# Kernel tuning notes

Hardware: AMD Instinct MI355X
Metric: run time of the kernel (lower is better)

The kernel has to match this reference:

```python
import jax, jax.numpy as jnp
import numpy as np

N, C_IN, C_HID, C_OUT = 50000, 256, 64 * 4, 64
E = 1_600_000
P_DROP = 0.5


def setup_inputs() -> dict:
    key = jax.random.key(0)
    ks = jax.random.split(key, 12)
    cat = C_IN + C_HID  # DConv input is concat([X, H]) -> in+hidden channels
    glorot = lambda k, sh: jax.random.normal(k, sh, jnp.float32) * (2.0 / (sh[-2] + sh[-1])) ** 0.5
    inp = {
        "x": jax.random.normal(ks[0], (N, C_IN), jnp.float32),
        "edge_index": jax.random.randint(ks[1], (2, E), 0, N, jnp.int64),
        "edge_weight": jax.random.uniform(ks[2], (E,), jnp.float32),
        # deterministic dropout mask (training-mode dropout, p=0.5), pre-scaled by 1/(1-p)
        "mask": (jax.random.uniform(ks[3], (N, C_IN)) >= P_DROP).astype(jnp.float32) / (1.0 - P_DROP),
        # DConv weights: shape (2, K=1, in+hidden, hidden) per gate
        "w_z": glorot(ks[4], (2, 1, cat, C_HID)),
        "b_z": jnp.zeros((C_HID,), jnp.float32),
        "w_r": glorot(ks[5], (2, 1, cat, C_HID)),
        "b_r": jnp.zeros((C_HID,), jnp.float32),
        "w_h": glorot(ks[6], (2, 1, cat, C_HID)),
        "b_h": jnp.zeros((C_HID,), jnp.float32),
        "w_lin": glorot(ks[7], (C_OUT, C_HID)),
        "b_lin": jnp.zeros((C_OUT,), jnp.float32),
    }
    return inp


def _dconv(inp, w, b):
    # K=1 diffusion conv: only the zeroth-order (identity) term of both the
    # forward- and backward-transition expansions survives; edges are unused.
    return inp @ w[0, 0] + inp @ w[1, 0] + b


def reference(x, edge_index, edge_weight, mask, w_z, b_z, w_r, b_r, w_h, b_h, w_lin, b_lin):
    x = x * mask  # F.dropout, training=True, deterministic mask
    H = jnp.zeros((x.shape[0], w_z.shape[-1]), x.dtype)  # initial hidden state
    xh = jnp.concatenate([x, H], axis=1)                  # [N, in+hid]
    Z = jax.nn.sigmoid(_dconv(xh, w_z, b_z))              # update gate
    R = jax.nn.sigmoid(_dconv(xh, w_r, b_r))              # reset gate
    xhr = jnp.concatenate([x, H * R], axis=1)
    H_tilde = jnp.tanh(_dconv(xhr, w_h, b_h))             # candidate state
    H = Z * H + (1.0 - Z) * H_tilde                       # GRU blend
    h = jax.nn.elu(H)
    return h @ w_lin.T + b_lin                            # [N, out]
```

## Files before the change

kernel.cpp:

```cpp
#include <hip/hip_runtime.h>
#include <hip/hip_bf16.h>


typedef __attribute__((ext_vector_type(8))) short bf16x8;
typedef __attribute__((ext_vector_type(4))) float f32x4;

constexpr int N_ROWS = 50000;
constexpr int CIN  = 256;
constexpr int COUT = 64;
constexpr int BM   = 32;

__device__ inline unsigned short f2bf(float f) {
    union { float f; unsigned u; } v; v.f = f;
    unsigned r = v.u + 0x7fffu + ((v.u >> 16) & 1u);
    return (unsigned short)(r >> 16);
}
__device__ inline float bf2f(unsigned short b) {
    union { unsigned u; float f; } v; v.u = ((unsigned)b) << 16;
    return v.f;
}
__device__ inline f32x4 mfma16(bf16x8 a, bf16x8 b, f32x4 c) {
    return __builtin_amdgcn_mfma_f32_16x16x32_bf16(a, b, c, 0, 0, 0);
}
__device__ __forceinline__ void gload16(const void* g, void* l) {
    __builtin_amdgcn_global_load_lds(
        (const __attribute__((address_space(1))) char*)g,
        (__attribute__((address_space(3))) char*)l, 16, 0, 0);
}

__global__ __launch_bounds__(256) void prep_frags(
    const float* __restrict__ wz, const float* __restrict__ wh,
    const float* __restrict__ wlin, unsigned short* __restrict__ ws)
{
    int t = blockIdx.x * 256 + threadIdx.x;
    int frag = t >> 6, lane = t & 63;
    if (frag >= 288) return;
    int g16 = lane & 15, kg = lane >> 4;
    unsigned short vals[8];
    if (frag < 256) {
        int kb = frag & 7, nf = (frag >> 3) & 15, g = frag >> 7;
        const float* wsrc = g ? wh : wz;
        int n = nf * 16 + g16;
        #pragma unroll
        for (int j = 0; j < 8; ++j) {
            int k = kb * 32 + kg * 8 + j;
            float v = wsrc[k * 256 + n] + wsrc[131072 + k * 256 + n];
            vals[j] = f2bf(v);
        }
    } else {
        int f = frag - 256;
        int kb = f & 7, nf = f >> 3;
        int n = nf * 16 + g16;
        #pragma unroll
        for (int j = 0; j < 8; ++j) {
            int k = kb * 32 + kg * 8 + j;
            vals[j] = f2bf(wlin[n * 256 + k]);
        }
    }
    unsigned short* dst = ws + (size_t)frag * 512 + lane * 8;
    #pragma unroll
    for (int j = 0; j < 8; ++j) dst[j] = vals[j];
}

__global__ __launch_bounds__(512)
__attribute__((amdgpu_waves_per_eu(4, 4)))
void dcrnn_async(
    const float* __restrict__ x, const float* __restrict__ mask,
    const unsigned short* __restrict__ wf,
    const float* __restrict__ bz, const float* __restrict__ bh,
    const float* __restrict__ blin, float* __restrict__ out)
{
    __shared__ char smem[65536];
    char* AhiB = smem;
    char* AloB = smem + 16384;
    const int tid = threadIdx.x, lane = tid & 63, wv = tid >> 6;
    const int l16 = lane & 15, lk = lane >> 4;
    const int row0 = blockIdx.x * BM;
    const int nf0 = wv * 2;
    char* wbuf = smem + 32768 + wv * 4096;

    auto stage_gate = [&](int kb, int g) {
        char* dst = wbuf + g * 2048;
        gload16(wf + (size_t)((g * 16 + nf0)     * 8 + kb) * 512 + lane * 8, dst);
        gload16(wf + (size_t)((g * 16 + nf0 + 1) * 8 + kb) * 512 + lane * 8, dst + 1024);
    };
    auto stage_out = [&](int v) {
        char* dst = wbuf + (v & 1) * 2048;
        gload16(wf + (size_t)(256 + (wv & 3) * 8 + 2 * v)     * 512 + lane * 8, dst);
        gload16(wf + (size_t)(256 + (wv & 3) * 8 + 2 * v + 1) * 512 + lane * 8, dst + 1024);
    };

    stage_gate(0, 0);
    stage_gate(0, 1);

    float bzv[2], bhv[2];
    #pragma unroll
    for (int nfi = 0; nfi < 2; ++nfi) {
        int col = wv * 32 + nfi * 16 + l16;
        bzv[nfi] = bz[col]; bhv[nfi] = bh[col];
    }
    const int ocol = (wv & 3) * 16 + l16;
    const float bo = blin[ocol];
    const int mo = wv >> 2;

    #pragma unroll
    for (int it = 0; it < 4; ++it) {
        int s = it * 512 + tid, r = s >> 6, c4 = s & 63;
        int row = row0 + r;
        float4 xv = make_float4(0.f, 0.f, 0.f, 0.f), mv = xv;
        if (row < N_ROWS) {
            xv = reinterpret_cast<const float4*>(x    + (size_t)row * CIN)[c4];
            mv = reinterpret_cast<const float4*>(mask + (size_t)row * CIN)[c4];
        }
        float v0 = xv.x * mv.x, v1 = xv.y * mv.y, v2 = xv.z * mv.z, v3 = xv.w * mv.w;
        unsigned short h0 = f2bf(v0), h1 = f2bf(v1), h2 = f2bf(v2), h3 = f2bf(v3);
        unsigned short l0 = f2bf(v0 - bf2f(h0)), l1 = f2bf(v1 - bf2f(h1));
        unsigned short l2 = f2bf(v2 - bf2f(h2)), l3 = f2bf(v3 - bf2f(h3));
        int byte = ((r * CIN + c4 * 4) * 2) ^ ((r & 7) << 4);
        *reinterpret_cast<ushort4*>(AhiB + byte) = make_ushort4(h0, h1, h2, h3);
        *reinterpret_cast<ushort4*>(AloB + byte) = make_ushort4(l0, l1, l2, l3);
    }
    __syncthreads();

    f32x4 accZ[2][2], accH[2][2];
    #pragma unroll
    for (int nfi = 0; nfi < 2; ++nfi)
        #pragma unroll
        for (int m = 0; m < 2; ++m) {
            accZ[nfi][m] = (f32x4){0.f, 0.f, 0.f, 0.f};
            accH[nfi][m] = (f32x4){0.f, 0.f, 0.f, 0.f};
        }

    for (int kb = 0; kb < 8; ++kb) {
        bf16x8 ah[2], al[2];
        int koff = kb * 32 + lk * 8;
        #pragma unroll
        for (int m = 0; m < 2; ++m) {
            int row = m * 16 + l16;
            int byte = ((row * CIN + koff) * 2) ^ ((row & 7) << 4);
            ah[m] = *reinterpret_cast<const bf16x8*>(AhiB + byte);
            al[m] = *reinterpret_cast<const bf16x8*>(AloB + byte);
        }
        if (kb >= 1) asm volatile("s_waitcnt vmcnt(2)" ::: "memory");
        bf16x8 zb0 = *reinterpret_cast<const bf16x8*>(wbuf + lane * 16);
        bf16x8 zb1 = *reinterpret_cast<const bf16x8*>(wbuf + 1024 + lane * 16);
        asm volatile("s_waitcnt lgkmcnt(0)" ::: "memory");
        if (kb < 7) stage_gate(kb + 1, 0); else stage_out(0);
        #pragma unroll
        for (int m = 0; m < 2; ++m) {
            accZ[0][m] = mfma16(ah[m], zb0, accZ[0][m]);
            accZ[0][m] = mfma16(al[m], zb0, accZ[0][m]);
            accZ[1][m] = mfma16(ah[m], zb1, accZ[1][m]);
            accZ[1][m] = mfma16(al[m], zb1, accZ[1][m]);
        }
        if (kb >= 1) asm volatile("s_waitcnt vmcnt(2)" ::: "memory");
        bf16x8 hb0 = *reinterpret_cast<const bf16x8*>(wbuf + 2048 + lane * 16);
        bf16x8 hb1 = *reinterpret_cast<const bf16x8*>(wbuf + 3072 + lane * 16);
        asm volatile("s_waitcnt lgkmcnt(0)" ::: "memory");
        if (kb < 7) stage_gate(kb + 1, 1); else stage_out(1);
        #pragma unroll
        for (int m = 0; m < 2; ++m) {
            accH[0][m] = mfma16(ah[m], hb0, accH[0][m]);
            accH[0][m] = mfma16(al[m], hb0, accH[0][m]);
            accH[1][m] = mfma16(ah[m], hb1, accH[1][m]);
            accH[1][m] = mfma16(al[m], hb1, accH[1][m]);
        }
    }
    __syncthreads();

    #pragma unroll
    for (int nfi = 0; nfi < 2; ++nfi) {
        int col = wv * 32 + nfi * 16 + l16;
        #pragma unroll
        for (int m = 0; m < 2; ++m) {
            #pragma unroll
            for (int i = 0; i < 4; ++i) {
                float z  = 1.f / (1.f + __expf(-(accZ[nfi][m][i] + bzv[nfi])));
                float tt = __expf(2.f * (accH[nfi][m][i] + bhv[nfi]));
                float th = (tt - 1.f) / (tt + 1.f);
                float H  = (1.f - z) * th;
                float h  = (H > 0.f) ? H : (__expf(H) - 1.f);
                int row = m * 16 + lk * 4 + i;
                unsigned pk = ((unsigned)f2bf(h)) << 16;
                int byte = (row * 1024 + col * 4) ^ ((row & 7) << 4);
                *reinterpret_cast<unsigned*>(smem + byte) = pk;
            }
        }
    }
    __syncthreads();

    f32x4 accO = (f32x4){0.f, 0.f, 0.f, 0.f};
    for (int v = 0; v < 4; ++v) {
        if (v == 2) asm volatile("s_waitcnt vmcnt(2)" ::: "memory");
        if (v == 3) asm volatile("s_waitcnt vmcnt(0)" ::: "memory");
        bf16x8 cb0 = *reinterpret_cast<const bf16x8*>(wbuf + (v & 1) * 2048 + lane * 16);
        bf16x8 cb1 = *reinterpret_cast<const bf16x8*>(wbuf + (v & 1) * 2048 + 1024 + lane * 16);
        asm volatile("s_waitcnt lgkmcnt(0)" ::: "memory");
        if (v < 2) stage_out(v + 2);
        #pragma unroll
        for (int j = 0; j < 2; ++j) {
            int kb = 2 * v + j;
            int row = mo * 16 + l16;
            int e0  = kb * 32 + lk * 8;
            int b0  = (row * 1024 + e0 * 4)      ^ ((row & 7) << 4);
            int b1  = (row * 1024 + e0 * 4 + 16) ^ ((row & 7) << 4);
            uint4 p0 = *reinterpret_cast<const uint4*>(smem + b0);
            uint4 p1 = *reinterpret_cast<const uint4*>(smem + b1);
            bf16x8 ha;
            ha[0] = (short)(p0.x >> 16); ha[1] = (short)(p0.y >> 16);
            ha[2] = (short)(p0.z >> 16); ha[3] = (short)(p0.w >> 16);
            ha[4] = (short)(p1.x >> 16); ha[5] = (short)(p1.y >> 16);
            ha[6] = (short)(p1.z >> 16); ha[7] = (short)(p1.w >> 16);
            accO = mfma16(ha, j ? cb1 : cb0, accO);
        }
    }
    #pragma unroll
    for (int i = 0; i < 4; ++i) {
        int row = row0 + mo * 16 + lk * 4 + i;
        if (row < N_ROWS) out[(size_t)row * COUT + ocol] = accO[i] + bo;
    }
}

__global__ __launch_bounds__(256) void fallback_f32(
    const float* __restrict__ x, const float* __restrict__ mask,
    const float* __restrict__ wzr, const float* __restrict__ whr,
    const float* __restrict__ bz, const float* __restrict__ bh,
    const float* __restrict__ wlinr, const float* __restrict__ blin,
    float* __restrict__ out)
{
    __shared__ float xm[32][CIN];
    const int tid = threadIdx.x;
    const int row0 = blockIdx.x * 32;
    #pragma unroll
    for (int it = 0; it < 8; ++it) {
        int idx = it * 256 + tid;
        int r = idx >> 6, c4 = idx & 63, row = row0 + r;
        float4 v = make_float4(0.f, 0.f, 0.f, 0.f);
        if (row < N_ROWS) {
            float4 a = reinterpret_cast<const float4*>(x    + (size_t)row * CIN)[c4];
            float4 m = reinterpret_cast<const float4*>(mask + (size_t)row * CIN)[c4];
            v = make_float4(a.x * m.x, a.y * m.y, a.z * m.z, a.w * m.w);
        }
        reinterpret_cast<float4*>(&xm[r][0])[c4] = v;
    }
    __syncthreads();
    const int j0 = (tid & 63) * 4, r0 = (tid >> 6) * 8;
    float accz[4][8], acch[4][8];
    #pragma unroll
    for (int c = 0; c < 4; ++c)
        #pragma unroll
        for (int r = 0; r < 8; ++r) { accz[c][r] = 0.f; acch[c][r] = 0.f; }
    for (int k = 0; k < CIN; k += 4) {
        float4 wz4[4], wh4[4];
        #pragma unroll
        for (int kk = 0; kk < 4; ++kk) {
            float4 a0 = *reinterpret_cast<const float4*>(&wzr[(k + kk) * 256 + j0]);
            float4 a1 = *reinterpret_cast<const float4*>(&wzr[131072 + (k + kk) * 256 + j0]);
            wz4[kk] = make_float4(a0.x + a1.x, a0.y + a1.y, a0.z + a1.z, a0.w + a1.w);
            float4 b0 = *reinterpret_cast<const float4*>(&whr[(k + kk) * 256 + j0]);
            float4 b1 = *reinterpret_cast<const float4*>(&whr[131072 + (k + kk) * 256 + j0]);
            wh4[kk] = make_float4(b0.x + b1.x, b0.y + b1.y, b0.z + b1.z, b0.w + b1.w);
        }
        #pragma unroll
        for (int r = 0; r < 8; ++r) {
            float4 xv = *reinterpret_cast<const float4*>(&xm[r0 + r][k]);
            float xk[4] = {xv.x, xv.y, xv.z, xv.w};
            float wzc[4][4] = {{wz4[0].x,wz4[0].y,wz4[0].z,wz4[0].w},{wz4[1].x,wz4[1].y,wz4[1].z,wz4[1].w},
                               {wz4[2].x,wz4[2].y,wz4[2].z,wz4[2].w},{wz4[3].x,wz4[3].y,wz4[3].z,wz4[3].w}};
            float whc[4][4] = {{wh4[0].x,wh4[0].y,wh4[0].z,wh4[0].w},{wh4[1].x,wh4[1].y,wh4[1].z,wh4[1].w},
                               {wh4[2].x,wh4[2].y,wh4[2].z,wh4[2].w},{wh4[3].x,wh4[3].y,wh4[3].z,wh4[3].w}};
            #pragma unroll
            for (int kk = 0; kk < 4; ++kk)
                #pragma unroll
                for (int c = 0; c < 4; ++c) {
                    accz[c][r] = fmaf(xk[kk], wzc[kk][c], accz[c][r]);
                    acch[c][r] = fmaf(xk[kk], whc[kk][c], acch[c][r]);
                }
        }
    }
    float bzj[4], bhj[4];
    #pragma unroll
    for (int c = 0; c < 4; ++c) { bzj[c] = bz[j0 + c]; bhj[c] = bh[j0 + c]; }
    __syncthreads();
    #pragma unroll
    for (int r = 0; r < 8; ++r) {
        float hc[4];
        #pragma unroll
        for (int c = 0; c < 4; ++c) {
            float z  = 1.f / (1.f + expf(-(accz[c][r] + bzj[c])));
            float ht = tanhf(acch[c][r] + bhj[c]);
            float H  = (1.f - z) * ht;
            hc[c] = (H > 0.f) ? H : expm1f(H);
        }
        *reinterpret_cast<float4*>(&xm[r0 + r][j0]) = make_float4(hc[0], hc[1], hc[2], hc[3]);
    }
    __syncthreads();
    const int o = tid & 63;
    float acc[8];
    #pragma unroll
    for (int r = 0; r < 8; ++r) acc[r] = 0.f;
    for (int k = 0; k < CIN; k += 4) {
        float4 wv4 = *reinterpret_cast<const float4*>(&wlinr[o * 256 + k]);
        #pragma unroll
        for (int r = 0; r < 8; ++r) {
            float4 hv = *reinterpret_cast<const float4*>(&xm[r0 + r][k]);
            acc[r] = fmaf(hv.x, wv4.x, acc[r]);
            acc[r] = fmaf(hv.y, wv4.y, acc[r]);
            acc[r] = fmaf(hv.z, wv4.z, acc[r]);
            acc[r] = fmaf(hv.w, wv4.w, acc[r]);
        }
    }
    float bo = blin[o];
    #pragma unroll
    for (int r = 0; r < 8; ++r) {
        int row = row0 + r0 + r;
        if (row < N_ROWS) out[(size_t)row * COUT + o] = acc[r] + bo;
    }
}

extern "C" void kernel_launch(void* const* d_in, const int* in_sizes, int n_in,
                              void* d_out, int out_size, void* d_ws, size_t ws_size,
                              hipStream_t stream)
{
    const float* x    = (const float*)d_in[0];
    const float* mask = (const float*)d_in[3];
    const float* wz   = (const float*)d_in[4];
    const float* bz   = (const float*)d_in[5];
    const float* wh   = (const float*)d_in[8];
    const float* bh   = (const float*)d_in[9];
    const float* wlin = (const float*)d_in[10];
    const float* blin = (const float*)d_in[11];
    float* outf = (float*)d_out;

    const size_t ws_need = 288 * 1024;
    if (ws_size >= ws_need) {
        unsigned short* wsf = (unsigned short*)d_ws;
        prep_frags<<<72, 256, 0, stream>>>(wz, wh, wlin, wsf);
        dcrnn_async<<<(N_ROWS + BM - 1) / BM, 512, 0, stream>>>(
            x, mask, wsf, bz, bh, blin, outf);
    } else {
        fallback_f32<<<(N_ROWS + 31) / 32, 256, 0, stream>>>(
            x, mask, wz, wh, bz, bh, wlin, blin, outf);
    }
}
```

Baseline: 61.68 us.

## Drop bf16 hi/lo split of inputs and load output weights directly from global

Removes the compensated lo-part of the bf16 input split, which halves the gate MFMAs, the LDS traffic and the A-tile shared memory. LDS shrinks from 64KB to 48KB and waves_per_eu is raised from 4 to 6 to allow more resident waves. The output-projection weights are now loaded straight from global into registers with one-ahead prefetch, instead of being staged through LDS. The cost is reduced precision on the input operand, since x*mask is now a single bf16 value.

```diff
diff --git a/kernel.cpp b/kernel.cpp
--- a/kernel.cpp
+++ b/kernel.cpp
@@ -14,10 +14,6 @@
     union { float f; unsigned u; } v; v.f = f;
     unsigned r = v.u + 0x7fffu + ((v.u >> 16) & 1u);
     return (unsigned short)(r >> 16);
-}
-__device__ inline float bf2f(unsigned short b) {
-    union { unsigned u; float f; } v; v.u = ((unsigned)b) << 16;
-    return v.f;
 }
 __device__ inline f32x4 mfma16(bf16x8 a, bf16x8 b, f32x4 c) {
     return __builtin_amdgcn_mfma_f32_16x16x32_bf16(a, b, c, 0, 0, 0);
@@ -62,32 +58,30 @@
     for (int j = 0; j < 8; ++j) dst[j] = vals[j];
 }
 
+__device__ inline bf16x8 ldfrag(const unsigned short* wf, int frag, int lane) {
+    return *reinterpret_cast<const bf16x8*>(wf + (size_t)frag * 512 + lane * 8);
+}
+
 __global__ __launch_bounds__(512)
-__attribute__((amdgpu_waves_per_eu(4, 4)))
+__attribute__((amdgpu_waves_per_eu(6, 6)))
 void dcrnn_async(
     const float* __restrict__ x, const float* __restrict__ mask,
     const unsigned short* __restrict__ wf,
     const float* __restrict__ bz, const float* __restrict__ bh,
     const float* __restrict__ blin, float* __restrict__ out)
 {
-    __shared__ char smem[65536];
+    __shared__ char smem[49152];
     char* AhiB = smem;
-    char* AloB = smem + 16384;
     const int tid = threadIdx.x, lane = tid & 63, wv = tid >> 6;
     const int l16 = lane & 15, lk = lane >> 4;
     const int row0 = blockIdx.x * BM;
     const int nf0 = wv * 2;
-    char* wbuf = smem + 32768 + wv * 4096;
+    char* wbuf = smem + 16384 + wv * 4096;
 
     auto stage_gate = [&](int kb, int g) {
         char* dst = wbuf + g * 2048;
         gload16(wf + (size_t)((g * 16 + nf0)     * 8 + kb) * 512 + lane * 8, dst);
         gload16(wf + (size_t)((g * 16 + nf0 + 1) * 8 + kb) * 512 + lane * 8, dst + 1024);
-    };
-    auto stage_out = [&](int v) {
-        char* dst = wbuf + (v & 1) * 2048;
-        gload16(wf + (size_t)(256 + (wv & 3) * 8 + 2 * v)     * 512 + lane * 8, dst);
-        gload16(wf + (size_t)(256 + (wv & 3) * 8 + 2 * v + 1) * 512 + lane * 8, dst + 1024);
     };
 
     stage_gate(0, 0);
@@ -112,13 +106,10 @@
             xv = reinterpret_cast<const float4*>(x    + (size_t)row * CIN)[c4];
             mv = reinterpret_cast<const float4*>(mask + (size_t)row * CIN)[c4];
         }
-        float v0 = xv.x * mv.x, v1 = xv.y * mv.y, v2 = xv.z * mv.z, v3 = xv.w * mv.w;
-        unsigned short h0 = f2bf(v0), h1 = f2bf(v1), h2 = f2bf(v2), h3 = f2bf(v3);
-        unsigned short l0 = f2bf(v0 - bf2f(h0)), l1 = f2bf(v1 - bf2f(h1));
-        unsigned short l2 = f2bf(v2 - bf2f(h2)), l3 = f2bf(v3 - bf2f(h3));
+        unsigned short h0 = f2bf(xv.x * mv.x), h1 = f2bf(xv.y * mv.y);
+        unsigned short h2 = f2bf(xv.z * mv.z), h3 = f2bf(xv.w * mv.w);
         int byte = ((r * CIN + c4 * 4) * 2) ^ ((r & 7) << 4);
         *reinterpret_cast<ushort4*>(AhiB + byte) = make_ushort4(h0, h1, h2, h3);
-        *reinterpret_cast<ushort4*>(AloB + byte) = make_ushort4(l0, l1, l2, l3);
     }
     __syncthreads();
 
@@ -132,40 +123,37 @@
         }
 
     for (int kb = 0; kb < 8; ++kb) {
-        bf16x8 ah[2], al[2];
+        bf16x8 ah[2];
         int koff = kb * 32 + lk * 8;
         #pragma unroll
         for (int m = 0; m < 2; ++m) {
             int row = m * 16 + l16;
             int byte = ((row * CIN + koff) * 2) ^ ((row & 7) << 4);
             ah[m] = *reinterpret_cast<const bf16x8*>(AhiB + byte);
-            al[m] = *reinterpret_cast<const bf16x8*>(AloB + byte);
         }
         if (kb >= 1) asm volatile("s_waitcnt vmcnt(2)" ::: "memory");
         bf16x8 zb0 = *reinterpret_cast<const bf16x8*>(wbuf + lane * 16);
         bf16x8 zb1 = *reinterpret_cast<const bf16x8*>(wbuf + 1024 + lane * 16);
         asm volatile("s_waitcnt lgkmcnt(0)" ::: "memory");
-        if (kb < 7) stage_gate(kb + 1, 0); else stage_out(0);
+        if (kb < 7) stage_gate(kb + 1, 0);
         #pragma unroll
         for (int m = 0; m < 2; ++m) {
             accZ[0][m] = mfma16(ah[m], zb0, accZ[0][m]);
-            accZ[0][m] = mfma16(al[m], zb0, accZ[0][m]);
             accZ[1][m] = mfma16(ah[m], zb1, accZ[1][m]);
-            accZ[1][m] = mfma16(al[m], zb1, accZ[1][m]);
-        }
-        if (kb >= 1) asm volatile("s_waitcnt vmcnt(2)" ::: "memory");
+        }
+        if (kb == 7)      asm volatile("s_waitcnt vmcnt(0)" ::: "memory");
+        else if (kb >= 1) asm volatile("s_waitcnt vmcnt(2)" ::: "memory");
         bf16x8 hb0 = *reinterpret_cast<const bf16x8*>(wbuf + 2048 + lane * 16);
         bf16x8 hb1 = *reinterpret_cast<const bf16x8*>(wbuf + 3072 + lane * 16);
         asm volatile("s_waitcnt lgkmcnt(0)" ::: "memory");
-        if (kb < 7) stage_gate(kb + 1, 1); else stage_out(1);
+        if (kb < 7) stage_gate(kb + 1, 1);
         #pragma unroll
         for (int m = 0; m < 2; ++m) {
             accH[0][m] = mfma16(ah[m], hb0, accH[0][m]);
-            accH[0][m] = mfma16(al[m], hb0, accH[0][m]);
             accH[1][m] = mfma16(ah[m], hb1, accH[1][m]);
-            accH[1][m] = mfma16(al[m], hb1, accH[1][m]);
-        }
-    }
+        }
+    }
+    bf16x8 cb = ldfrag(wf, 256 + (wv & 3) * 8, lane);
     __syncthreads();
 
     #pragma unroll
@@ -190,29 +178,22 @@
     __syncthreads();
 
     f32x4 accO = (f32x4){0.f, 0.f, 0.f, 0.f};
-    for (int v = 0; v < 4; ++v) {
-        if (v == 2) asm volatile("s_waitcnt vmcnt(2)" ::: "memory");
-        if (v == 3) asm volatile("s_waitcnt vmcnt(0)" ::: "memory");
-        bf16x8 cb0 = *reinterpret_cast<const bf16x8*>(wbuf + (v & 1) * 2048 + lane * 16);
-        bf16x8 cb1 = *reinterpret_cast<const bf16x8*>(wbuf + (v & 1) * 2048 + 1024 + lane * 16);
-        asm volatile("s_waitcnt lgkmcnt(0)" ::: "memory");
-        if (v < 2) stage_out(v + 2);
-        #pragma unroll
-        for (int j = 0; j < 2; ++j) {
-            int kb = 2 * v + j;
-            int row = mo * 16 + l16;
-            int e0  = kb * 32 + lk * 8;
-            int b0  = (row * 1024 + e0 * 4)      ^ ((row & 7) << 4);
-            int b1  = (row * 1024 + e0 * 4 + 16) ^ ((row & 7) << 4);
-            uint4 p0 = *reinterpret_cast<const uint4*>(smem + b0);
-            uint4 p1 = *reinterpret_cast<const uint4*>(smem + b1);
-            bf16x8 ha;
-            ha[0] = (short)(p0.x >> 16); ha[1] = (short)(p0.y >> 16);
-            ha[2] = (short)(p0.z >> 16); ha[3] = (short)(p0.w >> 16);
-            ha[4] = (short)(p1.x >> 16); ha[5] = (short)(p1.y >> 16);
-            ha[6] = (short)(p1.z >> 16); ha[7] = (short)(p1.w >> 16);
-            accO = mfma16(ha, j ? cb1 : cb0, accO);
-        }
+    for (int kb = 0; kb < 8; ++kb) {
+        int nk = kb < 7 ? kb + 1 : 7;
+        bf16x8 nb = ldfrag(wf, 256 + (wv & 3) * 8 + nk, lane);
+        int row = mo * 16 + l16;
+        int e0  = kb * 32 + lk * 8;
+        int b0  = (row * 1024 + e0 * 4)      ^ ((row & 7) << 4);
+        int b1  = (row * 1024 + e0 * 4 + 16) ^ ((row & 7) << 4);
+        uint4 p0 = *reinterpret_cast<const uint4*>(smem + b0);
+        uint4 p1 = *reinterpret_cast<const uint4*>(smem + b1);
+        bf16x8 ha;
+        ha[0] = (short)(p0.x >> 16); ha[1] = (short)(p0.y >> 16);
+        ha[2] = (short)(p0.z >> 16); ha[3] = (short)(p0.w >> 16);
+        ha[4] = (short)(p1.x >> 16); ha[5] = (short)(p1.y >> 16);
+        ha[6] = (short)(p1.z >> 16); ha[7] = (short)(p1.w >> 16);
+        accO = mfma16(ha, cb, accO);
+        cb = nb;
     }
     #pragma unroll
     for (int i = 0; i < 4; ++i) {
```

Result: faster. 56.97 us (-7.6%).
